# Performance work log

Measured on AMD Instinct MI355X. Metric: run time of the kernel, lower is better.

The kernel has to match this reference:

```python
import jax, jax.numpy as jnp
import numpy as np

B, N, DIM = 1, 4096, 512
HEADS, LOCAL_HEADS = 8, 4           # int(8*0.6)=4 local, 4 content
CONTENT_HEADS = HEADS - LOCAL_HEADS
HEAD_DIM = DIM // HEADS             # 64
WINDOW = 64                         # == H == W so window attention is well-formed
TOPK_RATIO = 0.2
SCALE = HEAD_DIM ** -0.5


def _window_partition(x, ws):
    Bb, H, W, C = x.shape
    pad_h = (ws - H % ws) % ws
    pad_w = (ws - W % ws) % ws
    x = jnp.pad(x, ((0, 0), (0, pad_h), (0, pad_w), (0, 0)))
    Hp, Wp = H + pad_h, W + pad_w
    x = x.reshape(Bb, Hp // ws, ws, Wp // ws, ws, C)
    win = x.transpose(0, 1, 3, 2, 4, 5).reshape(-1, ws, ws, C)
    return win, (Hp, Wp)


def _window_unpartition(win, ws, pad_hw, hw):
    Hp, Wp = pad_hw
    H, W = hw
    Bb = win.shape[0] // (Hp * Wp // ws // ws)
    x = win.reshape(Bb, Hp // ws, Wp // ws, ws, ws, -1)
    x = x.transpose(0, 1, 3, 2, 4, 5).reshape(Bb, Hp, Wp, -1)
    return x[:, :H, :W, :]


def setup_inputs() -> dict:
    key = jax.random.key(0)
    ks = jax.random.split(key, 12)
    s = 0.02
    f32 = jnp.float32
    ld = LOCAL_HEADS * HEAD_DIM      # 256
    cd = CONTENT_HEADS * HEAD_DIM    # 256
    return {
        'x': jax.random.normal(ks[0], (B, N, DIM), f32),
        'W_lqkv': jax.random.normal(ks[1], (DIM, 3 * ld), f32) * s,
        'b_lqkv': jnp.zeros((3 * ld,), f32),
        'W_cqkv': jax.random.normal(ks[2], (DIM, 3 * cd), f32) * s,
        'b_cqkv': jnp.zeros((3 * cd,), f32),
        'W_lproj': jax.random.normal(ks[3], (ld, DIM), f32) * s,
        'b_lproj': jnp.zeros((DIM,), f32),
        'W_cproj': jax.random.normal(ks[4], (cd, DIM), f32) * s,
        'b_cproj': jnp.zeros((DIM,), f32),
        'W_s1': jax.random.normal(ks[5], (DIM, DIM // 2), f32) * s,
        'b_s1': jnp.zeros((DIM // 2,), f32),
        'W_s2': jax.random.normal(ks[6], (DIM // 2, 1), f32) * s,
        'b_s2': jnp.zeros((1,), f32),
    }


def reference(x, W_lqkv, b_lqkv, W_cqkv, b_cqkv, W_lproj, b_lproj,
              W_cproj, b_cproj, W_s1, b_s1, W_s2, b_s2):
    Bb, Nn, C = x.shape
    H = W = int(np.sqrt(Nn))

    # ---- local (windowed) attention branch ----
    x_sp = x.reshape(Bb, H, W, C)
    x_win, pad_hw = _window_partition(x_sp, WINDOW)           # (Bw, ws, ws, C)
    Bw, Hw, Ww, _ = x_win.shape
    Nw = Hw * Ww
    xl = x_win.reshape(Bw, Nw, C)
    lqkv = (xl @ W_lqkv + b_lqkv).reshape(Bw, Nw, 3, LOCAL_HEADS, HEAD_DIM)
    lqkv = lqkv.transpose(2, 0, 3, 1, 4)                      # (3, Bw, h, Nw, d)
    lq, lk, lv = lqkv[0], lqkv[1], lqkv[2]
    lattn = jnp.einsum('bhqd,bhkd->bhqk', lq, lk) * SCALE
    lattn = jax.nn.softmax(lattn, axis=-1)
    lo = jnp.einsum('bhqk,bhkd->bhqd', lattn, lv)
    lo = lo.transpose(0, 2, 1, 3).reshape(Bw, Hw, Ww, LOCAL_HEADS * HEAD_DIM)
    lo = _window_unpartition(lo, WINDOW, pad_hw, (H, W)).reshape(Bb, Nn, -1)
    local_x = lo @ W_lproj + b_lproj

    # ---- saliency-gated content-based sparse attention branch ----
    h = jax.nn.gelu(x @ W_s1 + b_s1, approximate=False)
    scores = (h @ W_s2 + b_s2)[..., 0]                        # (B, N)
    K = max(1, int(Nn * TOPK_RATIO))
    _, idx = jax.lax.top_k(scores, K)                         # (B, K)
    mask = jnp.zeros((Bb, Nn), bool).at[jnp.arange(Bb)[:, None], idx].set(True)

    cqkv = (x @ W_cqkv + b_cqkv).reshape(Bb, Nn, 3, CONTENT_HEADS, HEAD_DIM)
    cqkv = cqkv.transpose(2, 0, 3, 1, 4)
    cq, ck, cv = cqkv[0], cqkv[1], cqkv[2]
    cattn = jnp.einsum('bhqd,bhkd->bhqk', cq, ck) * SCALE
    cattn = jnp.where(mask[:, None, None, :], cattn, -jnp.inf)
    cattn = jax.nn.softmax(cattn, axis=-1)
    co = jnp.einsum('bhqk,bhkd->bhqd', cattn, cv)
    co = co.transpose(0, 2, 1, 3).reshape(Bb, Nn, CONTENT_HEADS * HEAD_DIM)
    content_x = co @ W_cproj + b_cproj

    out = local_x + content_x
    attn = jnp.concatenate([lattn.mean(axis=1), cattn.mean(axis=1)], axis=1)
    return out, attn
```

## Files before the change

### kernel.cpp

```cpp
#include <hip/hip_runtime.h>

typedef __bf16 bf16;
typedef __bf16 bf16x4 __attribute__((ext_vector_type(4)));
typedef __bf16 bf16x8 __attribute__((ext_vector_type(8)));
typedef float  floatx4 __attribute__((ext_vector_type(4)));

__device__ __forceinline__ floatx4 mfma16(bf16x8 a, bf16x8 b, floatx4 c) {
    return __builtin_amdgcn_mfma_f32_16x16x32_bf16(a, b, c, 0, 0, 0);
}

__device__ __forceinline__ void transpose_tile(const float* __restrict__ src,
                                               bf16* __restrict__ dst,
                                               int R, int C, int rt, int ct,
                                               float (*tile)[33]) {
    int t = threadIdx.x;
    int tx = t & 31, ty = t >> 5;
    int c0 = ct * 32, r0 = rt * 32;
    for (int i = ty; i < 32; i += 8) {
        int r = r0 + i, c = c0 + tx;
        tile[i][tx] = (r < R && c < C) ? src[r * C + c] : 0.f;
    }
    __syncthreads();
    for (int i = ty; i < 32; i += 8) {
        int r = r0 + tx, c = c0 + i;
        if (r < R && c < C) dst[(size_t)c * R + r] = (bf16)tile[tx][i];
    }
}

__global__ __launch_bounds__(256) void k_prep(
    const float* __restrict__ W_lqkv, const float* __restrict__ W_cqkv,
    const float* __restrict__ x,
    bf16* __restrict__ WlT, bf16* __restrict__ WcT, bf16* __restrict__ xb)
{
    __shared__ float tile[32][33];
    int b = blockIdx.x;
    if (b < 384) {
        transpose_tile(W_lqkv, WlT, 512, 768, b / 24, b % 24, tile);
    } else if (b < 768) {
        transpose_tile(W_cqkv, WcT, 512, 768, (b - 384) / 24, (b - 384) % 24, tile);
    } else {
        int i = ((b - 768) * 256 + threadIdx.x) * 8;
        float4 f0 = *(const float4*)(x + i);
        float4 f1 = *(const float4*)(x + i + 4);
        bf16x8 a;
        a[0] = (bf16)f0.x; a[1] = (bf16)f0.y; a[2] = (bf16)f0.z; a[3] = (bf16)f0.w;
        a[4] = (bf16)f1.x; a[5] = (bf16)f1.y; a[6] = (bf16)f1.z; a[7] = (bf16)f1.w;
        *(bf16x8*)(xb + i) = a;
    }
}

__global__ __launch_bounds__(256) void k_qkv(
    const bf16* __restrict__ xb,
    const bf16* __restrict__ WlT, const bf16* __restrict__ WcT,
    const float* __restrict__ b_l, const float* __restrict__ b_c,
    bf16* __restrict__ lq, bf16* __restrict__ lk, bf16* __restrict__ lv,
    bf16* __restrict__ cq, bf16* __restrict__ ck, bf16* __restrict__ cv)
{
    const int tid = threadIdx.x;
    const int wave = tid >> 6, lane = tid & 63;
    const int ln15 = lane & 15, quad = lane >> 4;
    const int m0 = blockIdx.x * 64 + wave * 16;
    const int n0 = blockIdx.y * 64;

    floatx4 acc[4];
    for (int s = 0; s < 4; ++s) acc[s] = (floatx4){0.f, 0.f, 0.f, 0.f};

    for (int k0 = 0; k0 < 512; k0 += 32) {
        bf16x8 a = *(const bf16x8*)(xb + (m0 + ln15) * 512 + k0 + quad * 8);
        for (int s = 0; s < 4; ++s) {
            int cg = n0 + s * 16 + ln15;
            const bf16* bt = (cg < 768) ? (WlT + cg * 512) : (WcT + (cg - 768) * 512);
            bf16x8 b = *(const bf16x8*)(bt + k0 + quad * 8);
            acc[s] = mfma16(a, b, acc[s]);
        }
    }

    for (int s = 0; s < 4; ++s) {
        int cg = n0 + s * 16 + ln15;
        for (int r = 0; r < 4; ++r) {
            int row = m0 + quad * 4 + r;
            float v = acc[s][r];
            if (cg < 768) {
                v += b_l[cg];
                int qkv = cg >> 8, hh = (cg >> 6) & 3, d = cg & 63;
                if (qkv == 0)      lq[(hh * 4096 + row) * 64 + d] = (bf16)(v * 0.125f);
                else if (qkv == 1) lk[(hh * 4096 + row) * 64 + d] = (bf16)v;
                else               lv[(hh * 4096 + row) * 64 + d] = (bf16)v;
            } else {
                int c = cg - 768;
                v += b_c[c];
                int qkv = c >> 8, hh = (c >> 6) & 3, d = c & 63;
                if (qkv == 0)      cq[(hh * 4096 + row) * 64 + d] = (bf16)(v * 0.125f);
                else if (qkv == 1) ck[(hh * 4096 + row) * 64 + d] = (bf16)v;
                else               cv[(hh * 4096 + row) * 64 + d] = (bf16)v;
            }
        }
    }
}

__global__ __launch_bounds__(256) void k_scores(
    const float* __restrict__ x, const float* __restrict__ Ws1,
    const float* __restrict__ bs1, const float* __restrict__ Ws2,
    const float* __restrict__ bs2, float* __restrict__ scores)
{
    __shared__ float xs[16][512];
    int row0 = blockIdx.x * 16;
    int t = threadIdx.x;
    for (int i = t; i < 2048; i += 256) {
        int r = i >> 7, k4 = (i & 127) * 4;
        *(float4*)&xs[r][k4] = *(const float4*)&x[(row0 + r) * 512 + k4];
    }
    __syncthreads();
    int w = t >> 6, cb = (t & 63) * 4;
    float acc[4][4];
    #pragma unroll
    for (int rr = 0; rr < 4; ++rr)
        for (int j = 0; j < 4; ++j) acc[rr][j] = 0.f;
    #pragma unroll 2
    for (int k = 0; k < 512; ++k) {
        float4 wv = *(const float4*)(Ws1 + k * 256 + cb);
        #pragma unroll
        for (int rr = 0; rr < 4; ++rr) {
            float a = xs[w * 4 + rr][k];
            acc[rr][0] = fmaf(a, wv.x, acc[rr][0]);
            acc[rr][1] = fmaf(a, wv.y, acc[rr][1]);
            acc[rr][2] = fmaf(a, wv.z, acc[rr][2]);
            acc[rr][3] = fmaf(a, wv.w, acc[rr][3]);
        }
    }
    float b1[4] = {bs1[cb], bs1[cb + 1], bs1[cb + 2], bs1[cb + 3]};
    float w2[4] = {Ws2[cb], Ws2[cb + 1], Ws2[cb + 2], Ws2[cb + 3]};
    #pragma unroll
    for (int rr = 0; rr < 4; ++rr) {
        float s = 0.f;
        #pragma unroll
        for (int j = 0; j < 4; ++j) {
            float v = acc[rr][j] + b1[j];
            float g = 0.5f * v * (1.0f + erff(v * 0.70710678118654752f));
            s = fmaf(g, w2[j], s);
        }
        s += __shfl_xor(s, 1, 64);  s += __shfl_xor(s, 2, 64);
        s += __shfl_xor(s, 4, 64);  s += __shfl_xor(s, 8, 64);
        s += __shfl_xor(s, 16, 64); s += __shfl_xor(s, 32, 64);
        if ((t & 63) == 0) scores[row0 + w * 4 + rr] = s + bs2[0];
    }
}

__global__ __launch_bounds__(1024) void k_topk(const float* __restrict__ scores,
                                               int* __restrict__ sel, int* __restrict__ pos) {
    __shared__ unsigned ubuf[4096];
    __shared__ unsigned cga[2048], cgb[2048];
    __shared__ int bidx[1024];
    __shared__ int ctr, bctr, Bbin;
    int tid = threadIdx.x;
    if (tid == 0) { ctr = 0; bctr = 0; }
    for (int i = tid; i < 2048; i += 1024) cga[i] = 0u;
    __syncthreads();
    for (int i = tid; i < 4096; i += 1024) {
        unsigned s = __float_as_uint(scores[i]);
        unsigned u = (s & 0x80000000u) ? ~s : (s | 0x80000000u);
        ubuf[i] = u;
        pos[i] = -1;
        atomicAdd(&cga[u >> 21], 1u);
    }
    __syncthreads();
    unsigned* src = cga; unsigned* dst = cgb;
    for (int off = 1; off < 2048; off <<= 1) {
        for (int i = tid; i < 2048; i += 1024)
            dst[i] = src[i] + ((i + off < 2048) ? src[i + off] : 0u);
        __syncthreads();
        unsigned* tmp = src; src = dst; dst = tmp;
    }
    for (int b = tid; b < 2048; b += 1024) {
        unsigned ge = src[b];
        unsigned gt = (b < 2047) ? src[b + 1] : 0u;
        if (ge >= 819u && gt < 819u) Bbin = b;
    }
    __syncthreads();
    int B = Bbin;
    int countAbove = (B < 2047) ? (int)src[B + 1] : 0;
    int need = 819 - countAbove;
    for (int i = tid; i < 4096; i += 1024) {
        int b = (int)(ubuf[i] >> 21);
        if (b > B) {
            int slot = atomicAdd(&ctr, 1);
            sel[slot] = i;
            pos[i] = slot;
        } else if (b == B) {
            int ls = atomicAdd(&bctr, 1);
            if (ls < 1024) bidx[ls] = i;
        }
    }
    __syncthreads();
    int m = bctr;
    if (m <= 1024) {
        for (int e = tid; e < m; e += 1024) {
            int i = bidx[e];
            unsigned ui = ubuf[i];
            int rank = 0;
            for (int j = 0; j < m; ++j) {
                int ij = bidx[j];
                unsigned uj = ubuf[ij];
                rank += (uj > ui || (uj == ui && ij < i)) ? 1 : 0;
            }
            if (rank < need) { int slot = countAbove + rank; sel[slot] = i; pos[i] = slot; }
        }
    } else {
        for (int i = tid; i < 4096; i += 1024) {
            if ((int)(ubuf[i] >> 21) != B) continue;
            unsigned ui = ubuf[i];
            int rank = 0;
            for (int j = 0; j < 4096; ++j) {
                if ((int)(ubuf[j] >> 21) != B) continue;
                unsigned uj = ubuf[j];
                rank += (uj > ui || (uj == ui && j < i)) ? 1 : 0;
            }
            if (rank < need) { int slot = countAbove + rank; sel[slot] = i; pos[i] = slot; }
        }
    }
}

__global__ __launch_bounds__(256) void k_vt2(
    const bf16* __restrict__ lv, bf16* __restrict__ lvT,
    const bf16* __restrict__ ck, const bf16* __restrict__ cv,
    const int* __restrict__ sel,
    bf16* __restrict__ ckg, bf16* __restrict__ cvgT)
{
    __shared__ bf16 tile[64][66];
    int b = blockIdx.x;
    int t = threadIdx.x;
    int lane = t & 63, grp = t >> 6;
    if (b < 256) {
        int tr = b & 63, h = b >> 6;
        const bf16* s = lv + ((size_t)h * 4096 + tr * 64) * 64;
        #pragma unroll
        for (int rr = 0; rr < 16; ++rr) {
            int row = rr * 4 + grp;
            tile[row][lane] = s[row * 64 + lane];
        }
        __syncthreads();
        bf16* d = lvT + (size_t)h * 64 * 4096 + tr * 64;
        #pragma unroll
        for (int cc = 0; cc < 16; ++cc) {
            int col = cc * 4 + grp;
            d[(size_t)col * 4096 + lane] = tile[lane][col];
        }
    } else {
        int g = b - 256;
        int hh = g / 14, tl = g % 14;
        int r0 = tl * 64;
        #pragma unroll
        for (int rr = 0; rr < 16; ++rr) {
            int row = r0 + rr * 4 + grp;
            int src = (row < 819) ? sel[row] : -1;
            bf16 kv = (src >= 0) ? ck[(hh * 4096 + src) * 64 + lane] : (bf16)0.0f;
            bf16 vv = (src >= 0) ? cv[(hh * 4096 + src) * 64 + lane] : (bf16)0.0f;
            ckg[(hh * 896 + row) * 64 + lane] = kv;
            tile[rr * 4 + grp][lane] = vv;
        }
        __syncthreads();
        bf16* d = cvgT + (size_t)hh * 64 * 896 + r0;
        #pragma unroll
        for (int cc = 0; cc < 16; ++cc) {
            int col = cc * 4 + grp;
            d[(size_t)col * 896 + lane] = tile[lane][col];
        }
    }
}

__global__ __launch_bounds__(256, 5) void k_pass2b(
    const bf16* __restrict__ lq, const bf16* __restrict__ lk, const bf16* __restrict__ lvT,
    const bf16* __restrict__ cq, const bf16* __restrict__ ckg, const bf16* __restrict__ cvgT,
    float* __restrict__ partOL,
    float* __restrict__ partOC,
    float* __restrict__ partSL,
    float* __restrict__ partSC)
{
    __shared__ __align__(16) bf16 pbuf[4][2][16 * 40];
    int wave = threadIdx.x >> 6, lane = threadIdx.x & 63;
    int ln15 = lane & 15, quad = lane >> 4;
    int m0 = blockIdx.x * 64 + wave * 16;
    int y = blockIdx.y;
    bool local = y < 32;
    int h     = local ? (y >> 3) : ((y - 32) >> 1);
    int split = local ? (y & 7) : ((y - 32) & 1);
    int NV    = local ? 4096 : 896;
    int kbeg  = local ? split * 512 : split * 448;
    int kcnt  = local ? 512 : 448;

    const bf16* Qh = (local ? lq : cq) + (h * 4096 + m0) * 64;
    const bf16* Kh = (local ? lk : ckg) + h * NV * 64;
    const bf16* Vh = (local ? lvT : cvgT) + h * 64 * NV;

    bf16x8 af0 = *(const bf16x8*)(Qh + ln15 * 64 + quad * 8);
    bf16x8 af1 = *(const bf16x8*)(Qh + ln15 * 64 + 32 + quad * 8);

    floatx4 o[4];
    #pragma unroll
    for (int ds = 0; ds < 4; ++ds) o[ds] = (floatx4){0.f, 0.f, 0.f, 0.f};
    float se[4] = {0.f, 0.f, 0.f, 0.f};

    for (int key0 = kbeg; key0 < kbeg + kcnt; key0 += 64) {
        #pragma unroll
        for (int c = 0; c < 2; ++c) {
            int kb = key0 + c * 32;
            bf16* pb = &pbuf[wave][c][0];
            #pragma unroll
            for (int s = 0; s < 2; ++s) {
                int kc = kb + s * 16;
                const bf16* krow = Kh + (kc + ln15) * 64;
                floatx4 z0 = (floatx4){0.f, 0.f, 0.f, 0.f};
                floatx4 z1 = (floatx4){0.f, 0.f, 0.f, 0.f};
                z0 = mfma16(af0, *(const bf16x8*)(krow + quad * 8), z0);
                z1 = mfma16(af1, *(const bf16x8*)(krow + 32 + quad * 8), z1);
                bool valid = local || (kc + ln15) < 819;
                #pragma unroll
                for (int r = 0; r < 4; ++r) {
                    float p = valid ? __expf(fminf(z0[r] + z1[r], 60.f)) : 0.0f;
                    se[r] += p;
                    pb[(quad * 4 + r) * 40 + s * 16 + ln15] = (bf16)p;
                }
            }
        }
        #pragma unroll
        for (int c = 0; c < 2; ++c) {
            int kb = key0 + c * 32;
            bf16x8 ap = *(const bf16x8*)(&pbuf[wave][c][0] + ln15 * 40 + quad * 8);
            #pragma unroll
            for (int ds = 0; ds < 4; ++ds) {
                const bf16* vrow = Vh + (ds * 16 + ln15) * NV + kb + quad * 8;
                o[ds] = mfma16(ap, *(const bf16x8*)vrow, o[ds]);
            }
        }
    }

    float* ps = (local ? partSL : partSC) + (split * 4 + h) * 4096;
    #pragma unroll
    for (int r = 0; r < 4; ++r) {
        float s = se[r];
        s += __shfl_xor(s, 1, 64);
        s += __shfl_xor(s, 2, 64);
        s += __shfl_xor(s, 4, 64);
        s += __shfl_xor(s, 8, 64);
        if (ln15 == 0) ps[m0 + quad * 4 + r] = s;
    }

    float* ob = (local ? partOL : partOC) + (size_t)split * (4096 * 256);
    #pragma unroll
    for (int ds = 0; ds < 4; ++ds)
        for (int r = 0; r < 4; ++r)
            ob[(m0 + quad * 4 + r) * 256 + h * 64 + ds * 16 + ln15] = o[ds][r];
}

__global__ __launch_bounds__(256) void k_reduce2(
    const float* __restrict__ partOL, const float* __restrict__ partOC,
    const float* __restrict__ partSL, const float* __restrict__ partSC,
    float* __restrict__ lsum, bf16* __restrict__ lob, bf16* __restrict__ cob)
{
    int t = threadIdx.x;
    int q0 = blockIdx.x * 4;
    int r = t >> 6, cc = (t & 63) * 4;
    int q = q0 + r;
    int h = cc >> 6;

    float sl = 0.f;
    #pragma unroll
    for (int s = 0; s < 8; ++s) sl += partSL[(s * 4 + h) * 4096 + q];
    float rll = 1.0f / fmaxf(sl, 1e-30f);
    float a0 = 0.f, a1 = 0.f, a2 = 0.f, a3 = 0.f;
    #pragma unroll
    for (int s = 0; s < 8; ++s) {
        float4 v = *(const float4*)(partOL + (size_t)s * 1048576 + q * 256 + cc);
        a0 += v.x; a1 += v.y; a2 += v.z; a3 += v.w;
    }
    bf16x4 ol;
    ol[0] = (bf16)(a0 * rll); ol[1] = (bf16)(a1 * rll);
    ol[2] = (bf16)(a2 * rll); ol[3] = (bf16)(a3 * rll);
    *(bf16x4*)(lob + q * 256 + cc) = ol;

    float sc = partSC[h * 4096 + q] + partSC[(4 + h) * 4096 + q];
    float rlc = 1.0f / fmaxf(sc, 1e-30f);
    float4 v0 = *(const float4*)(partOC + q * 256 + cc);
    float4 v1 = *(const float4*)(partOC + 1048576 + q * 256 + cc);
    bf16x4 oc;
    oc[0] = (bf16)((v0.x + v1.x) * rlc); oc[1] = (bf16)((v0.y + v1.y) * rlc);
    oc[2] = (bf16)((v0.z + v1.z) * rlc); oc[3] = (bf16)((v0.w + v1.w) * rlc);
    *(bf16x4*)(cob + q * 256 + cc) = oc;

    if (t < 32) {
        int h8 = t >> 2, rr = t & 3, qq = q0 + rr;
        float s = 0.f;
        if (h8 < 4) {
            #pragma unroll
            for (int sp = 0; sp < 8; ++sp) s += partSL[(sp * 4 + h8) * 4096 + qq];
        } else {
            s = partSC[(h8 - 4) * 4096 + qq] + partSC[(4 + h8 - 4) * 4096 + qq];
        }
        lsum[h8 * 4096 + qq] = s;
    }
}

__global__ __launch_bounds__(256) void k_pass2a(
    const bf16* __restrict__ lq, const bf16* __restrict__ lk,
    const bf16* __restrict__ cq, const bf16* __restrict__ ckg,
    const float* __restrict__ lsum,
    float* __restrict__ attn_local,
    bf16* __restrict__ pcomp)
{
    int wave = threadIdx.x >> 6, lane = threadIdx.x & 63;
    int ln15 = lane & 15, quad = lane >> 4;
    int m0 = blockIdx.x * 64 + wave * 16;
    int y = blockIdx.y;
    bool local = y < 32;
    const bf16* Q  = local ? lq : cq;
    const bf16* Kt = local ? lk : ckg;
    int NV = local ? 4096 : 896;
    int kbeg = local ? y * 128 : (y - 32) * 128;
    int kend = kbeg + 128;
    int hbase = local ? 0 : 4;

    bf16x8 af[4][2];
    #pragma unroll
    for (int h2 = 0; h2 < 4; ++h2)
        for (int ks = 0; ks < 2; ++ks)
            af[h2][ks] = *(const bf16x8*)(Q + (h2 * 4096 + m0 + ln15) * 64 + ks * 32 + quad * 8);

    float rl[4][4];
    #pragma unroll
    for (int h2 = 0; h2 < 4; ++h2)
        for (int r = 0; r < 4; ++r)
            rl[h2][r] = 0.25f / fmaxf(lsum[(hbase + h2) * 4096 + m0 + quad * 4 + r], 1e-30f);

    for (int key0 = kbeg; key0 < kend; key0 += 32) {
        float pm[2][4] = {{0.f, 0.f, 0.f, 0.f}, {0.f, 0.f, 0.f, 0.f}};
        #pragma unroll
        for (int h2 = 0; h2 < 4; ++h2) {
            #pragma unroll
            for (int s = 0; s < 2; ++s) {
                int kc = key0 + s * 16;
                const bf16* krow = Kt + (h2 * NV + kc + ln15) * 64;
                floatx4 z0 = (floatx4){0.f, 0.f, 0.f, 0.f};
                floatx4 z1 = (floatx4){0.f, 0.f, 0.f, 0.f};
                z0 = mfma16(af[h2][0], *(const bf16x8*)(krow + quad * 8), z0);
                z1 = mfma16(af[h2][1], *(const bf16x8*)(krow + 32 + quad * 8), z1);
                bool valid = local || (kc + ln15) < 819;
                if (valid)
                    for (int r = 0; r < 4; ++r)
                        pm[s][r] += __expf(fminf(z0[r] + z1[r], 60.f)) * rl[h2][r];
            }
        }
        if (local) {
            #pragma unroll
            for (int s = 0; s < 2; ++s)
                for (int r = 0; r < 4; ++r)
                    attn_local[(m0 + quad * 4 + r) * 4096 + key0 + s * 16 + ln15] = pm[s][r];
        } else {
            #pragma unroll
            for (int s = 0; s < 2; ++s) {
                int kc = key0 + s * 16 + ln15;
                if (kc < 832)
                    for (int r = 0; r < 4; ++r)
                        pcomp[(m0 + quad * 4 + r) * 832 + kc] = (bf16)(pm[s][r]);
            }
        }
    }
}

__global__ __launch_bounds__(256) void k_expand2(
    const bf16* __restrict__ pcomp, const int* __restrict__ pos,
    const float* __restrict__ W_lproj, const float* __restrict__ W_cproj,
    bf16* __restrict__ WlpT, bf16* __restrict__ WcpT,
    float* __restrict__ attn_content)
{
    __shared__ float tile[32][33];
    int b = blockIdx.x;
    if (b < 4096) {
        int c0 = threadIdx.x * 16;
        const bf16* prow = pcomp + b * 832;
        float vals[16];
        #pragma unroll
        for (int j = 0; j < 16; ++j) {
            int p = pos[c0 + j];
            vals[j] = (p >= 0) ? (float)prow[p] : 0.0f;
        }
        float* dst = attn_content + (size_t)b * 4096 + c0;
        *(float4*)(dst)      = (float4){vals[0], vals[1], vals[2], vals[3]};
        *(float4*)(dst + 4)  = (float4){vals[4], vals[5], vals[6], vals[7]};
        *(float4*)(dst + 8)  = (float4){vals[8], vals[9], vals[10], vals[11]};
        *(float4*)(dst + 12) = (float4){vals[12], vals[13], vals[14], vals[15]};
    } else if (b < 4224) {
        int g = b - 4096;
        transpose_tile(W_lproj, WlpT, 256, 512, g / 16, g % 16, tile);
    } else {
        int g = b - 4224;
        transpose_tile(W_cproj, WcpT, 256, 512, g / 16, g % 16, tile);
    }
}

__global__ __launch_bounds__(256) void k_proj(
    const bf16* __restrict__ lob, const bf16* __restrict__ cob,
    const bf16* __restrict__ WlpT, const bf16* __restrict__ WcpT,
    const float* __restrict__ bl, const float* __restrict__ bc,
    float* __restrict__ out)
{
    const int tid = threadIdx.x;
    const int wave = tid >> 6, lane = tid & 63;
    const int ln15 = lane & 15, quad = lane >> 4;
    const int m0 = blockIdx.x * 64 + wave * 16;
    const int n0 = blockIdx.y * 32;

    floatx4 acc[2];
    acc[0] = (floatx4){0.f, 0.f, 0.f, 0.f};
    acc[1] = (floatx4){0.f, 0.f, 0.f, 0.f};

    for (int k0 = 0; k0 < 256; k0 += 32) {
        bf16x8 al = *(const bf16x8*)(lob + (m0 + ln15) * 256 + k0 + quad * 8);
        bf16x8 ac = *(const bf16x8*)(cob + (m0 + ln15) * 256 + k0 + quad * 8);
        #pragma unroll
        for (int s = 0; s < 2; ++s) {
            int c = n0 + s * 16 + ln15;
            acc[s] = mfma16(al, *(const bf16x8*)(WlpT + c * 256 + k0 + quad * 8), acc[s]);
            acc[s] = mfma16(ac, *(const bf16x8*)(WcpT + c * 256 + k0 + quad * 8), acc[s]);
        }
    }
    #pragma unroll
    for (int s = 0; s < 2; ++s) {
        int c = n0 + s * 16 + ln15;
        float bias = bl[c] + bc[c];
        for (int r = 0; r < 4; ++r)
            out[(m0 + quad * 4 + r) * 512 + c] = acc[s][r] + bias;
    }
}

#define OFF_WLQKVT  0L
#define OFF_WCQKVT  786432L
#define OFF_LQ      1572864L
#define OFF_LK      3670016L
#define OFF_LVT     5767168L
#define OFF_CQ      7864320L
#define OFF_CK      9961472L
#define OFF_CV      12058624L
#define OFF_PCOMP   9961472L
#define OFF_CKG     16777216L
#define OFF_CVGT    17235968L
#define OFF_WLPT    16777216L
#define OFF_WCPT    17039360L
#define OFF_SCORES  17694720L
#define OFF_SEL     17711104L
#define OFF_POS     17715200L
#define OFF_LSUM    17731584L
#define OFF_LO      17862656L
#define OFF_CO      22056960L
#define WS_TOTAL    26251264L

extern "C" void kernel_launch(void* const* d_in, const int* in_sizes, int n_in,
                              void* d_out, int out_size, void* d_ws, size_t ws_size,
                              hipStream_t stream) {
    if (ws_size < (size_t)WS_TOTAL) return;

    const float* x       = (const float*)d_in[0];
    const float* W_lqkv  = (const float*)d_in[1];
    const float* b_lqkv  = (const float*)d_in[2];
    const float* W_cqkv  = (const float*)d_in[3];
    const float* b_cqkv  = (const float*)d_in[4];
    const float* W_lproj = (const float*)d_in[5];
    const float* b_lproj = (const float*)d_in[6];
    const float* W_cproj = (const float*)d_in[7];
    const float* b_cproj = (const float*)d_in[8];
    const float* W_s1    = (const float*)d_in[9];
    const float* b_s1    = (const float*)d_in[10];
    const float* W_s2    = (const float*)d_in[11];
    const float* b_s2    = (const float*)d_in[12];

    char* ws = (char*)d_ws;
    bf16* WlqkvT  = (bf16*)(ws + OFF_WLQKVT);
    bf16* WcqkvT  = (bf16*)(ws + OFF_WCQKVT);
    bf16* lq    = (bf16*)(ws + OFF_LQ);
    bf16* lk    = (bf16*)(ws + OFF_LK);
    bf16* lvT   = (bf16*)(ws + OFF_LVT);
    bf16* cq    = (bf16*)(ws + OFF_CQ);
    bf16* ck    = (bf16*)(ws + OFF_CK);
    bf16* cv    = (bf16*)(ws + OFF_CV);
    bf16* pcomp = (bf16*)(ws + OFF_PCOMP);
    bf16* ckg   = (bf16*)(ws + OFF_CKG);
    bf16* cvgT  = (bf16*)(ws + OFF_CVGT);
    bf16* WlpT  = (bf16*)(ws + OFF_WLPT);
    bf16* WcpT  = (bf16*)(ws + OFF_WCPT);
    float* scores  = (float*)(ws + OFF_SCORES);
    int*   sel     = (int*)(ws + OFF_SEL);
    int*   pos     = (int*)(ws + OFF_POS);
    float* lsum    = (float*)(ws + OFF_LSUM);
    bf16*  xb      = (bf16*)(ws + OFF_LO);
    bf16*  lob     = (bf16*)(ws + OFF_LO);
    bf16*  lv      = (bf16*)(ws + OFF_CO);
    bf16*  cob     = (bf16*)(ws + OFF_CO);

    float* outp = (float*)d_out;
    float* attn_local   = outp + 2097152;
    float* attn_content = attn_local + 4096 * 4096;
    float* partOL = attn_content;
    float* partOC = attn_content + 8388608;
    float* partSL = attn_content + 10485760;
    float* partSC = attn_content + 10616832;

    k_prep<<<1792, 256, 0, stream>>>(W_lqkv, W_cqkv, x, WlqkvT, WcqkvT, xb);
    k_qkv<<<dim3(64, 24), 256, 0, stream>>>(xb, WlqkvT, WcqkvT, b_lqkv, b_cqkv,
                                            lq, lk, lv, cq, ck, cv);
    k_scores<<<256, 256, 0, stream>>>(x, W_s1, b_s1, W_s2, b_s2, scores);
    k_topk<<<1, 1024, 0, stream>>>(scores, sel, pos);
    k_vt2<<<312, 256, 0, stream>>>(lv, lvT, ck, cv, sel, ckg, cvgT);
    k_pass2b<<<dim3(64, 40), 256, 0, stream>>>(lq, lk, lvT, cq, ckg, cvgT,
                                               partOL, partOC, partSL, partSC);
    k_reduce2<<<1024, 256, 0, stream>>>(partOL, partOC, partSL, partSC, lsum, lob, cob);
    k_pass2a<<<dim3(64, 39), 256, 0, stream>>>(lq, lk, cq, ckg, lsum,
                                               attn_local, pcomp);
    k_expand2<<<4352, 256, 0, stream>>>(pcomp, pos, W_lproj, W_cproj,
                                        WlpT, WcpT, attn_content);
    k_proj<<<dim3(64, 16), 256, 0, stream>>>(lob, cob, WlpT, WcpT, b_lproj, b_cproj, outp);
}
```

Before: 679.8 us.

## Halve key-split count in attention passes and normalize content output in-kernel

Reduces the key-dimension split in pass2b from 8 to 4 for local heads and from 2 to 1 for content heads. Content blocks now normalize and write bf16 output and row sums directly, which removes the content partial buffers and their reduction. pass2a is regridded from 39 to 20 y-blocks, each covering a larger key range. This cuts partial-sum traffic and reduction work, but launches fewer blocks, so occupancy and load balance may suffer on a 256-CU device.

```diff
diff --git a/kernel.cpp b/kernel.cpp
--- a/kernel.cpp
+++ b/kernel.cpp
@@ -272,21 +272,21 @@
     const bf16* __restrict__ lq, const bf16* __restrict__ lk, const bf16* __restrict__ lvT,
     const bf16* __restrict__ cq, const bf16* __restrict__ ckg, const bf16* __restrict__ cvgT,
     float* __restrict__ partOL,
-    float* __restrict__ partOC,
     float* __restrict__ partSL,
-    float* __restrict__ partSC)
+    float* __restrict__ lsum,
+    bf16* __restrict__ cob)
 {
     __shared__ __align__(16) bf16 pbuf[4][2][16 * 40];
     int wave = threadIdx.x >> 6, lane = threadIdx.x & 63;
     int ln15 = lane & 15, quad = lane >> 4;
     int m0 = blockIdx.x * 64 + wave * 16;
     int y = blockIdx.y;
-    bool local = y < 32;
-    int h     = local ? (y >> 3) : ((y - 32) >> 1);
-    int split = local ? (y & 7) : ((y - 32) & 1);
+    bool local = y < 16;
+    int h     = local ? (y >> 2) : (y - 16);
+    int split = local ? (y & 3) : 0;
     int NV    = local ? 4096 : 896;
-    int kbeg  = local ? split * 512 : split * 448;
-    int kcnt  = local ? 512 : 448;
+    int kbeg  = local ? split * 1024 : 0;
+    int kcnt  = local ? 1024 : 896;
 
     const bf16* Qh = (local ? lq : cq) + (h * 4096 + m0) * 64;
     const bf16* Kh = (local ? lk : ckg) + h * NV * 64;
@@ -334,28 +334,45 @@
         }
     }
 
-    float* ps = (local ? partSL : partSC) + (split * 4 + h) * 4096;
-    #pragma unroll
-    for (int r = 0; r < 4; ++r) {
-        float s = se[r];
-        s += __shfl_xor(s, 1, 64);
-        s += __shfl_xor(s, 2, 64);
-        s += __shfl_xor(s, 4, 64);
-        s += __shfl_xor(s, 8, 64);
-        if (ln15 == 0) ps[m0 + quad * 4 + r] = s;
-    }
-
-    float* ob = (local ? partOL : partOC) + (size_t)split * (4096 * 256);
-    #pragma unroll
-    for (int ds = 0; ds < 4; ++ds)
-        for (int r = 0; r < 4; ++r)
-            ob[(m0 + quad * 4 + r) * 256 + h * 64 + ds * 16 + ln15] = o[ds][r];
+    if (local) {
+        float* ps = partSL + (split * 4 + h) * 4096;
+        #pragma unroll
+        for (int r = 0; r < 4; ++r) {
+            float s = se[r];
+            s += __shfl_xor(s, 1, 64);
+            s += __shfl_xor(s, 2, 64);
+            s += __shfl_xor(s, 4, 64);
+            s += __shfl_xor(s, 8, 64);
+            if (ln15 == 0) ps[m0 + quad * 4 + r] = s;
+        }
+        float* ob = partOL + (size_t)split * (4096 * 256);
+        #pragma unroll
+        for (int ds = 0; ds < 4; ++ds)
+            for (int r = 0; r < 4; ++r)
+                ob[(m0 + quad * 4 + r) * 256 + h * 64 + ds * 16 + ln15] = o[ds][r];
+    } else {
+        float rl[4];
+        #pragma unroll
+        for (int r = 0; r < 4; ++r) {
+            float s = se[r];
+            s += __shfl_xor(s, 1, 64);
+            s += __shfl_xor(s, 2, 64);
+            s += __shfl_xor(s, 4, 64);
+            s += __shfl_xor(s, 8, 64);
+            if (ln15 == 0) lsum[(4 + h) * 4096 + m0 + quad * 4 + r] = s;
+            rl[r] = 1.0f / fmaxf(s, 1e-30f);
+        }
+        #pragma unroll
+        for (int ds = 0; ds < 4; ++ds)
+            for (int r = 0; r < 4; ++r)
+                cob[(m0 + quad * 4 + r) * 256 + h * 64 + ds * 16 + ln15] =
+                    (bf16)(o[ds][r] * rl[r]);
+    }
 }
 
 __global__ __launch_bounds__(256) void k_reduce2(
-    const float* __restrict__ partOL, const float* __restrict__ partOC,
-    const float* __restrict__ partSL, const float* __restrict__ partSC,
-    float* __restrict__ lsum, bf16* __restrict__ lob, bf16* __restrict__ cob)
+    const float* __restrict__ partOL, const float* __restrict__ partSL,
+    float* __restrict__ lsum, bf16* __restrict__ lob)
 {
     int t = threadIdx.x;
     int q0 = blockIdx.x * 4;
@@ -365,11 +382,11 @@
 
     float sl = 0.f;
     #pragma unroll
-    for (int s = 0; s < 8; ++s) sl += partSL[(s * 4 + h) * 4096 + q];
+    for (int s = 0; s < 4; ++s) sl += partSL[(s * 4 + h) * 4096 + q];
     float rll = 1.0f / fmaxf(sl, 1e-30f);
     float a0 = 0.f, a1 = 0.f, a2 = 0.f, a3 = 0.f;
     #pragma unroll
-    for (int s = 0; s < 8; ++s) {
+    for (int s = 0; s < 4; ++s) {
         float4 v = *(const float4*)(partOL + (size_t)s * 1048576 + q * 256 + cc);
         a0 += v.x; a1 += v.y; a2 += v.z; a3 += v.w;
     }
@@ -378,24 +395,11 @@
     ol[2] = (bf16)(a2 * rll); ol[3] = (bf16)(a3 * rll);
     *(bf16x4*)(lob + q * 256 + cc) = ol;
 
-    float sc = partSC[h * 4096 + q] + partSC[(4 + h) * 4096 + q];
-    float rlc = 1.0f / fmaxf(sc, 1e-30f);
-    float4 v0 = *(const float4*)(partOC + q * 256 + cc);
-    float4 v1 = *(const float4*)(partOC + 1048576 + q * 256 + cc);
-    bf16x4 oc;
-    oc[0] = (bf16)((v0.x + v1.x) * rlc); oc[1] = (bf16)((v0.y + v1.y) * rlc);
-    oc[2] = (bf16)((v0.z + v1.z) * rlc); oc[3] = (bf16)((v0.w + v1.w) * rlc);
-    *(bf16x4*)(cob + q * 256 + cc) = oc;
-
-    if (t < 32) {
+    if (t < 16) {
         int h8 = t >> 2, rr = t & 3, qq = q0 + rr;
         float s = 0.f;
-        if (h8 < 4) {
-            #pragma unroll
-            for (int sp = 0; sp < 8; ++sp) s += partSL[(sp * 4 + h8) * 4096 + qq];
-        } else {
-            s = partSC[(h8 - 4) * 4096 + qq] + partSC[(4 + h8 - 4) * 4096 + qq];
-        }
+        #pragma unroll
+        for (int sp = 0; sp < 4; ++sp) s += partSL[(sp * 4 + h8) * 4096 + qq];
         lsum[h8 * 4096 + qq] = s;
     }
 }
@@ -411,12 +415,12 @@
     int ln15 = lane & 15, quad = lane >> 4;
     int m0 = blockIdx.x * 64 + wave * 16;
     int y = blockIdx.y;
-    bool local = y < 32;
+    bool local = y < 16;
     const bf16* Q  = local ? lq : cq;
     const bf16* Kt = local ? lk : ckg;
     int NV = local ? 4096 : 896;
-    int kbeg = local ? y * 128 : (y - 32) * 128;
-    int kend = kbeg + 128;
+    int kbeg = local ? y * 256 : (y - 16) * 224;
+    int kend = kbeg + (local ? 256 : 224);
     int hbase = local ? 0 : 4;
 
     bf16x8 af[4][2];
@@ -599,9 +603,7 @@
     float* attn_local   = outp + 2097152;
     float* attn_content = attn_local + 4096 * 4096;
     float* partOL = attn_content;
-    float* partOC = attn_content + 8388608;
-    float* partSL = attn_content + 10485760;
-    float* partSC = attn_content + 10616832;
+    float* partSL = attn_content + 4194304;
 
     k_prep<<<1792, 256, 0, stream>>>(W_lqkv, W_cqkv, x, WlqkvT, WcqkvT, xb);
     k_qkv<<<dim3(64, 24), 256, 0, stream>>>(xb, WlqkvT, WcqkvT, b_lqkv, b_cqkv,
@@ -609,10 +611,10 @@
     k_scores<<<256, 256, 0, stream>>>(x, W_s1, b_s1, W_s2, b_s2, scores);
     k_topk<<<1, 1024, 0, stream>>>(scores, sel, pos);
     k_vt2<<<312, 256, 0, stream>>>(lv, lvT, ck, cv, sel, ckg, cvgT);
-    k_pass2b<<<dim3(64, 40), 256, 0, stream>>>(lq, lk, lvT, cq, ckg, cvgT,
-                                               partOL, partOC, partSL, partSC);
-    k_reduce2<<<1024, 256, 0, stream>>>(partOL, partOC, partSL, partSC, lsum, lob, cob);
-    k_pass2a<<<dim3(64, 39), 256, 0, stream>>>(lq, lk, cq, ckg, lsum,
+    k_pass2b<<<dim3(64, 20), 256, 0, stream>>>(lq, lk, lvT, cq, ckg, cvgT,
+                                               partOL, partSL, lsum, cob);
+    k_reduce2<<<1024, 256, 0, stream>>>(partOL, partSL, lsum, lob);
+    k_pass2a<<<dim3(64, 20), 256, 0, stream>>>(lq, lk, cq, ckg, lsum,
                                                attn_local, pcomp);
     k_expand2<<<4352, 256, 0, stream>>>(pcomp, pos, W_lproj, W_cproj,
                                         WlpT, WcpT, attn_content);
```

Result: faster. 657.9 us (-3.2%).
